# Kernel tuning notes

Measured on AMD Instinct MI355X. Metric: run time of the kernel, lower is better.

## Reference

```python
import jax, jax.numpy as jnp
import numpy as np

WS = 49        # window size
NH = 8         # num heads


def setup_inputs() -> dict:
    key = jax.random.key(0)
    k1, k2, k3 = jax.random.split(key, 3)
    B, N, C = 4, 50176, 512
    x = jax.random.normal(k1, (B, N, C), dtype=jnp.float32)
    w_qkv = jax.random.normal(k2, (3 * C, C), dtype=jnp.float32) * (C ** -0.5)
    b_qkv = jnp.zeros((3 * C,), dtype=jnp.float32)
    w_proj = jax.random.normal(k3, (C, C), dtype=jnp.float32) * (C ** -0.5)
    b_proj = jnp.zeros((C,), dtype=jnp.float32)
    return {"x": x, "w_qkv": w_qkv, "b_qkv": b_qkv, "w_proj": w_proj, "b_proj": b_proj}


def reference(x, w_qkv, b_qkv, w_proj, b_proj):
    B, N, C = x.shape
    w = N // WS
    hd = C // NH
    scale = hd ** -0.5
    # shuffle: 'b (ws w) c -> (b w) ws c'  (outer factor is ws -> strided windows)
    xw = x.reshape(B, WS, w, C).transpose(0, 2, 1, 3).reshape(B * w, WS, C)
    qkv = xw @ w_qkv.T + b_qkv                       # [(B w), WS, 3C]
    qkv = qkv.reshape(B * w, WS, 3, NH, hd)
    q = qkv[:, :, 0].transpose(0, 2, 1, 3) * scale   # [(B w), NH, WS, hd]
    k = qkv[:, :, 1].transpose(0, 2, 1, 3)
    v = qkv[:, :, 2].transpose(0, 2, 1, 3)
    attn = jax.nn.softmax(jnp.einsum('bhqd,bhkd->bhqk', q, k), axis=-1)
    out = jnp.einsum('bhqk,bhkd->bhqd', attn, v)     # [(B w), NH, WS, hd]
    out = out.transpose(0, 2, 1, 3).reshape(B * w, WS, C)
    out = out @ w_proj.T + b_proj
    # unshuffle: '(b w) ws c -> b (ws w) c'
    out = out.reshape(B, w, WS, C).transpose(0, 2, 1, 3).reshape(B, N, C)
    return out
```

## Files before the change

kernel.cpp:

```cpp
#include <hip/hip_runtime.h>
#include <cstdint>
#include <cstddef>


typedef __bf16 bf16x8 __attribute__((ext_vector_type(8)));
typedef __bf16 bf16x4 __attribute__((ext_vector_type(4)));
typedef float  f32x4  __attribute__((ext_vector_type(4)));

#define MFMA_BF16(a, b, c) __builtin_amdgcn_mfma_f32_16x16x32_bf16((a), (b), (c), 0, 0, 0)

static __device__ __forceinline__ int swzi(int row, int col) {
  return col ^ ((row & 7) << 3);
}

typedef __attribute__((address_space(1))) const void gconst_t;
typedef __attribute__((address_space(3))) void lds_t;
static __device__ __forceinline__ void gload16(const void* g, void* l) {
  __builtin_amdgcn_global_load_lds((gconst_t*)g, (lds_t*)l, 16, 0, 0);
}

#define RAW_BAR()  asm volatile("s_barrier" ::: "memory")
#define WAITV(N)   asm volatile("s_waitcnt vmcnt(" #N ")" ::: "memory")

__global__ void prep_weights(const float* __restrict__ wqkv,
                             const float* __restrict__ bqkv,
                             const float* __restrict__ wproj,
                             __bf16* __restrict__ wqkv_bf,
                             __bf16* __restrict__ wproj_bf,
                             float* __restrict__ bq_s) {
  const int stride = gridDim.x * blockDim.x;
  const int t0 = blockIdx.x * blockDim.x + threadIdx.x;
  for (int i = t0; i < 1536 * 512; i += stride) {
    float v = wqkv[i];
    if (i < 512 * 512) v *= 0.125f;
    wqkv_bf[i] = (__bf16)v;
  }
  for (int i = t0; i < 512 * 512; i += stride) wproj_bf[i] = (__bf16)wproj[i];
  for (int i = t0; i < 1536; i += stride)      bq_s[i] = (i < 512 ? 0.125f : 1.0f) * bqkv[i];
}

__global__ void prep_x(const float* __restrict__ x, __bf16* __restrict__ xb) {
  const size_t total  = (size_t)200704 * 512 / 8;
  const size_t stride = (size_t)gridDim.x * blockDim.x;
  for (size_t i = (size_t)blockIdx.x * blockDim.x + threadIdx.x; i < total; i += stride) {
    const float4 a = *(const float4*)(x + i * 8);
    const float4 b = *(const float4*)(x + i * 8 + 4);
    bf16x8 t;
    t[0] = (__bf16)a.x; t[1] = (__bf16)a.y; t[2] = (__bf16)a.z; t[3] = (__bf16)a.w;
    t[4] = (__bf16)b.x; t[5] = (__bf16)b.y; t[6] = (__bf16)b.z; t[7] = (__bf16)b.w;
    *(bf16x8*)(xb + i * 8) = t;
  }
}

template<bool OUT_F32>
__launch_bounds__(512, 1)
__global__ void gemm256(const __bf16* __restrict__ Ab,
                        const __bf16* __restrict__ Bw,
                        const float* __restrict__ bias,
                        void* __restrict__ Cv,
                        int Mtiles, int Ntiles) {
  __shared__ __align__(16) __bf16 sA[2][256 * 64];
  __shared__ __align__(16) __bf16 sB[2][256 * 64];

  const int tid  = threadIdx.x;
  const int lane = tid & 63;
  const int l15  = lane & 15;
  const int kgc  = (lane >> 4) & 3;
  const int r4   = kgc * 4;
  const int wv   = tid >> 6;
  const int wm   = wv >> 2, wn = wv & 3;

  const int nwg = Mtiles * Ntiles;
  const int cpx = nwg >> 3;
  const int wg  = (blockIdx.x & 7) * cpx + (blockIdx.x >> 3);
  const int mt  = wg / Ntiles;
  const int nt  = wg % Ntiles;
  const size_t m0 = (size_t)mt * 256;
  const int    n0 = nt * 256;

  const int srow   = tid >> 3;
  const int schunk = (tid & 7) ^ (srow & 7);

  f32x4 acc[8][4];
  const f32x4 zf = {0.f, 0.f, 0.f, 0.f};
#pragma unroll
  for (int i = 0; i < 8; ++i)
#pragma unroll
    for (int j = 0; j < 4; ++j) acc[i][j] = zf;

  auto STAGE = [&](int bufi, int kt) {
    const size_t kof = (size_t)kt * 64 + schunk * 8;
#pragma unroll
    for (int j = 0; j < 4; ++j) {
      gload16(Ab + (m0 + (size_t)(j * 64 + srow)) * 512 + kof,
              &sA[bufi][0] + j * 4096 + tid * 8);
      gload16(Bw + ((size_t)(n0 + j * 64 + srow)) * 512 + kof,
              &sB[bufi][0] + j * 4096 + tid * 8);
    }
  };

  auto COMPUTE = [&](int bufi) {
#pragma unroll
    for (int ks = 0; ks < 2; ++ks) {
      bf16x8 bfrag[4];
#pragma unroll
      for (int n = 0; n < 4; ++n) {
        const int r = wn * 64 + n * 16 + l15;
        bfrag[n] = *(const bf16x8*)&sB[bufi][r * 64 + (((ks * 4 + kgc) ^ (r & 7)) * 8)];
      }
#pragma unroll
      for (int mh = 0; mh < 2; ++mh) {
        bf16x8 afrag[4];
#pragma unroll
        for (int m2 = 0; m2 < 4; ++m2) {
          const int r = wm * 128 + mh * 64 + m2 * 16 + l15;
          afrag[m2] = *(const bf16x8*)&sA[bufi][r * 64 + (((ks * 4 + kgc) ^ (r & 7)) * 8)];
        }
        __builtin_amdgcn_s_setprio(1);
#pragma unroll
        for (int m2 = 0; m2 < 4; ++m2)
#pragma unroll
          for (int n = 0; n < 4; ++n)
            acc[mh * 4 + m2][n] = MFMA_BF16(afrag[m2], bfrag[n], acc[mh * 4 + m2][n]);
        __builtin_amdgcn_s_setprio(0);
      }
    }
  };

  STAGE(0, 0);

  for (int tt = 0; tt < 8; tt += 2) {
    RAW_BAR();
    STAGE(1, tt + 1);
    WAITV(8);
    RAW_BAR();
    COMPUTE(0);

    RAW_BAR();
    if (tt < 6) {
      STAGE(0, tt + 2);
      WAITV(8);
    } else {
      WAITV(0);
    }
    RAW_BAR();
    COMPUTE(1);
  }

  const int Nld = Ntiles * 256;
#pragma unroll
  for (int n = 0; n < 4; ++n) {
    const int col = n0 + wn * 64 + n * 16 + l15;
    const float bb = bias[col];
#pragma unroll
    for (int m = 0; m < 8; ++m) {
#pragma unroll
      for (int r = 0; r < 4; ++r) {
        const size_t row = m0 + wm * 128 + m * 16 + r4 + r;
        const float v = acc[m][n][r] + bb;
        if (OUT_F32) ((float*)Cv)[row * (size_t)Nld + col] = v;
        else         ((__bf16*)Cv)[row * (size_t)Nld + col] = (__bf16)v;
      }
    }
  }
}

__launch_bounds__(512)
__global__ void attn_win(const __bf16* __restrict__ qkv, __bf16* __restrict__ O) {
  __shared__ __align__(16) __bf16 vT[8 * 64 * 64];
  __shared__ __align__(16) __bf16 sP[8][16 * 64];

  const int tid  = threadIdx.x;
  const int lane = tid & 63;
  const int h    = tid >> 6;
  const int l15  = lane & 15;
  const int kg   = ((lane >> 4) & 3) * 8;
  const int r4   = ((lane >> 4) & 3) * 4;

  const int blk = blockIdx.x;
  const int b   = blk >> 10;
  const int wi  = blk & 1023;
  const size_t tokbase = (size_t)b * 50176 + wi;

  const int MOFF[4] = {0, 16, 32, 33};
  const float NEG_INF = -__builtin_inff();

  bf16x8 aq[4][2], bk[4][2];
#pragma unroll
  for (int mt = 0; mt < 4; ++mt) {
    const size_t tok = tokbase + (size_t)(MOFF[mt] + l15) * 1024;
#pragma unroll
    for (int ks = 0; ks < 2; ++ks) {
      aq[mt][ks] = *(const bf16x8*)(qkv + tok * 1536 +       h * 64 + ks * 32 + kg);
      bk[mt][ks] = *(const bf16x8*)(qkv + tok * 1536 + 512 + h * 64 + ks * 32 + kg);
    }
  }

  for (int i = tid; i < 8 * 64 * 16; i += 512) {
    const int k = 48 + (i & 15);
    if (k != 48) {
      const int n  = (i >> 4) & 63;
      const int hh = i >> 10;
      vT[hh * 4096 + n * 64 + (k ^ ((n & 7) << 3))] = (__bf16)0.0f;
    }
  }
  for (int i = tid; i < 49 * 64; i += 512) {
    const int s  = i >> 6;
    const int c8 = (i & 63) * 8;
    bf16x8 v8 = *(const bf16x8*)(qkv + (tokbase + (size_t)s * 1024) * 1536 + 1024 + c8);
    const int hh = c8 >> 6;
#pragma unroll
    for (int j = 0; j < 8; ++j) {
      const int n = (c8 & 63) + j;
      vT[hh * 4096 + n * 64 + (s ^ ((n & 7) << 3))] = v8[j];
    }
  }
  __syncthreads();

  bf16x8 bv[4][2];
#pragma unroll
  for (int ntv = 0; ntv < 4; ++ntv) {
    const int n = ntv * 16 + l15;
#pragma unroll
    for (int ks = 0; ks < 2; ++ks)
      bv[ntv][ks] = *(const bf16x8*)&vT[h * 4096 + n * 64 + ((ks * 32 + kg) ^ ((n & 7) << 3))];
  }

  f32x4 accS[4][4];
  const f32x4 zf = {0.f, 0.f, 0.f, 0.f};
#pragma unroll
  for (int m = 0; m < 4; ++m)
#pragma unroll
    for (int n = 0; n < 4; ++n) accS[m][n] = zf;
#pragma unroll
  for (int ks = 0; ks < 2; ++ks)
#pragma unroll
    for (int m = 0; m < 4; ++m)
#pragma unroll
      for (int n = 0; n < 4; ++n)
        accS[m][n] = MFMA_BF16(aq[m][ks], bk[n][ks], accS[m][n]);

#pragma unroll
  for (int mt = 0; mt < 4; ++mt) {
#pragma unroll
    for (int r = 0; r < 4; ++r) {
      const int prow = r4 + r;
      const float sv0 = accS[mt][0][r];
      const float sv1 = accS[mt][1][r];
      const float sv2 = accS[mt][2][r];
      const float sv3 = (l15 == 15) ? accS[mt][3][r] : NEG_INF;
      float mx = fmaxf(fmaxf(sv0, sv1), fmaxf(sv2, sv3));
      mx = fmaxf(mx, __shfl_xor(mx, 1));
      mx = fmaxf(mx, __shfl_xor(mx, 2));
      mx = fmaxf(mx, __shfl_xor(mx, 4));
      mx = fmaxf(mx, __shfl_xor(mx, 8));
      const float e0 = __expf(sv0 - mx);
      const float e1 = __expf(sv1 - mx);
      const float e2 = __expf(sv2 - mx);
      const float e3 = __expf(sv3 - mx);
      float sum = e0 + e1 + e2 + e3;
      sum += __shfl_xor(sum, 1);
      sum += __shfl_xor(sum, 2);
      sum += __shfl_xor(sum, 4);
      sum += __shfl_xor(sum, 8);
      const float inv = 1.0f / sum;
      sP[h][prow * 64 + swzi(prow, 0  + l15)] = (__bf16)(e0 * inv);
      sP[h][prow * 64 + swzi(prow, 16 + l15)] = (__bf16)(e1 * inv);
      sP[h][prow * 64 + swzi(prow, 32 + l15)] = (__bf16)(e2 * inv);
      if (l15 == 15) sP[h][prow * 64 + swzi(prow, 48)] = (__bf16)(e3 * inv);
      if (l15 < 15)  sP[h][prow * 64 + swzi(prow, 49 + l15)] = (__bf16)0.0f;
    }
    bf16x8 ap[2];
#pragma unroll
    for (int ks = 0; ks < 2; ++ks)
      ap[ks] = *(const bf16x8*)&sP[h][l15 * 64 + swzi(l15, ks * 32 + kg)];
    f32x4 accO[4];
#pragma unroll
    for (int n = 0; n < 4; ++n) accO[n] = zf;
#pragma unroll
    for (int ks = 0; ks < 2; ++ks)
#pragma unroll
      for (int n = 0; n < 4; ++n)
        accO[n] = MFMA_BF16(ap[ks], bv[n][ks], accO[n]);
#pragma unroll
    for (int n = 0; n < 4; ++n) {
#pragma unroll
      for (int r = 0; r < 4; ++r) {
        const int row = MOFF[mt] + r4 + r;
        O[(tokbase + (size_t)row * 1024) * 512 + h * 64 + n * 16 + l15] =
            (__bf16)accO[n][r];
      }
    }
  }
}

__launch_bounds__(256, 2)
__global__ void swin_attn_fused(const float* __restrict__ x,
                                const __bf16* __restrict__ wqkv_bf,
                                const float* __restrict__ bq_s,
                                const __bf16* __restrict__ wproj_bf,
                                const float* __restrict__ bproj,
                                float* __restrict__ out) {
  __shared__ __align__(16) __bf16 s_xw[49 * 512];
  __shared__ __align__(16) __bf16 s_q [49 * 64];
  __shared__ __align__(16) __bf16 s_k [49 * 64];
  __shared__ __align__(16) __bf16 s_vT[64 * 64];
  __shared__ __align__(16) __bf16 s_p [49 * 64];

  const int tid  = threadIdx.x;
  const int lane = tid & 63;
  const int wv   = tid >> 6;
  const int l15  = lane & 15;
  const int kg   = (lane >> 4) * 8;
  const int r4   = (lane >> 4) * 4;
  const int blk = blockIdx.x;
  const int b   = blk >> 10;
  const int wi  = blk & 1023;
  const int MOFF[4] = {0, 16, 32, 33};
  const float NEG_INF = -__builtin_inff();

  for (int i = tid; i < 64 * 64; i += 256) s_vT[i] = (__bf16)0.0f;
  const float* xwin = x + ((size_t)b * 50176 + (size_t)wi) * 512;
  for (int idx = tid; idx < 49 * 128; idx += 256) {
    const int row = idx >> 7;
    const int c4  = (idx & 127) * 4;
    const float4 v = *(const float4*)(xwin + (size_t)row * (1024 * 512) + c4);
    bf16x4 t;
    t.x = (__bf16)v.x; t.y = (__bf16)v.y; t.z = (__bf16)v.z; t.w = (__bf16)v.w;
    *(bf16x4*)&s_xw[row * 512 + swzi(row, c4)] = t;
  }
  f32x4 accF[4][8];
  const f32x4 zf = {0.f, 0.f, 0.f, 0.f};
#pragma unroll
  for (int m = 0; m < 4; ++m)
#pragma unroll
    for (int n = 0; n < 8; ++n) accF[m][n] = zf;
  __syncthreads();

  for (int h = 0; h < 8; ++h) {
    f32x4 accA[4][3];
#pragma unroll
    for (int m = 0; m < 4; ++m)
#pragma unroll
      for (int n = 0; n < 3; ++n) accA[m][n] = zf;
    const __bf16* pB[3];
    float biasv[3];
#pragma unroll
    for (int nt = 0; nt < 3; ++nt) {
      const int c  = wv * 48 + nt * 16 + l15;
      const int wr = (c < 64) ? (h * 64 + c)
                   : (c < 128) ? (512 + h * 64 + (c - 64))
                               : (1024 + h * 64 + (c - 128));
      pB[nt]    = wqkv_bf + (size_t)wr * 512 + kg;
      biasv[nt] = bq_s[wr];
    }
#pragma unroll
    for (int ks = 0; ks < 16; ++ks) {
      bf16x8 a[4], bb[3];
#pragma unroll
      for (int mt = 0; mt < 4; ++mt) {
        const int row = MOFF[mt] + l15;
        a[mt] = *(const bf16x8*)&s_xw[row * 512 + swzi(row, ks * 32 + kg)];
      }
#pragma unroll
      for (int nt = 0; nt < 3; ++nt) bb[nt] = *(const bf16x8*)(pB[nt] + ks * 32);
#pragma unroll
      for (int mt = 0; mt < 4; ++mt)
#pragma unroll
        for (int nt = 0; nt < 3; ++nt)
          accA[mt][nt] = MFMA_BF16(a[mt], bb[nt], accA[mt][nt]);
    }
#pragma unroll
    for (int nt = 0; nt < 3; ++nt) {
      const int c = wv * 48 + nt * 16 + l15;
#pragma unroll
      for (int mt = 0; mt < 4; ++mt) {
#pragma unroll
        for (int r = 0; r < 4; ++r) {
          const int row = MOFF[mt] + r4 + r;
          const __bf16 bvv = (__bf16)(accA[mt][nt][r] + biasv[nt]);
          if (c < 64)       s_q[row * 64 + swzi(row, c)] = bvv;
          else if (c < 128) s_k[row * 64 + swzi(row, c - 64)] = bvv;
          else {
            const int vr = c - 128;
            s_vT[vr * 64 + swzi(vr, row)] = bvv;
          }
        }
      }
    }
    __syncthreads();

    const int R = MOFF[wv];
    bf16x8 aq[2], bkf[4][2];
#pragma unroll
    for (int ks2 = 0; ks2 < 2; ++ks2) {
      const int row = R + l15;
      aq[ks2] = *(const bf16x8*)&s_q[row * 64 + swzi(row, ks2 * 32 + kg)];
    }
#pragma unroll
    for (int nt = 0; nt < 4; ++nt) {
      const int row = MOFF[nt] + l15;
#pragma unroll
      for (int ks2 = 0; ks2 < 2; ++ks2)
        bkf[nt][ks2] = *(const bf16x8*)&s_k[row * 64 + swzi(row, ks2 * 32 + kg)];
    }
    f32x4 accS[4];
#pragma unroll
    for (int n = 0; n < 4; ++n) accS[n] = zf;
#pragma unroll
    for (int ks2 = 0; ks2 < 2; ++ks2)
#pragma unroll
      for (int nt = 0; nt < 4; ++nt)
        accS[nt] = MFMA_BF16(aq[ks2], bkf[nt][ks2], accS[nt]);
#pragma unroll
    for (int r = 0; r < 4; ++r) {
      const int row = R + r4 + r;
      const float sv0 = accS[0][r];
      const float sv1 = accS[1][r];
      const float sv2 = accS[2][r];
      const float sv3 = (l15 == 15) ? accS[3][r] : NEG_INF;
      float m = fmaxf(fmaxf(sv0, sv1), fmaxf(sv2, sv3));
      m = fmaxf(m, __shfl_xor(m, 1));
      m = fmaxf(m, __shfl_xor(m, 2));
      m = fmaxf(m, __shfl_xor(m, 4));
      m = fmaxf(m, __shfl_xor(m, 8));
      const float e0 = __expf(sv0 - m);
      const float e1 = __expf(sv1 - m);
      const float e2 = __expf(sv2 - m);
      const float e3 = __expf(sv3 - m);
      float s = e0 + e1 + e2 + e3;
      s += __shfl_xor(s, 1);
      s += __shfl_xor(s, 2);
      s += __shfl_xor(s, 4);
      s += __shfl_xor(s, 8);
      const float inv = 1.0f / s;
      s_p[row * 64 + swzi(row, 0  + l15)] = (__bf16)(e0 * inv);
      s_p[row * 64 + swzi(row, 16 + l15)] = (__bf16)(e1 * inv);
      s_p[row * 64 + swzi(row, 32 + l15)] = (__bf16)(e2 * inv);
      if (l15 == 15) s_p[row * 64 + swzi(row, 48)] = (__bf16)(e3 * inv);
      if (l15 < 15)  s_p[row * 64 + swzi(row, 49 + l15)] = (__bf16)0.0f;
    }
    bf16x8 ap[2], bv2[4][2];
#pragma unroll
    for (int ks2 = 0; ks2 < 2; ++ks2) {
      const int row = R + l15;
      ap[ks2] = *(const bf16x8*)&s_p[row * 64 + swzi(row, ks2 * 32 + kg)];
    }
#pragma unroll
    for (int nt = 0; nt < 4; ++nt) {
      const int row = nt * 16 + l15;
#pragma unroll
      for (int ks2 = 0; ks2 < 2; ++ks2)
        bv2[nt][ks2] = *(const bf16x8*)&s_vT[row * 64 + swzi(row, ks2 * 32 + kg)];
    }
    __syncthreads();
    f32x4 accO[4];
#pragma unroll
    for (int n = 0; n < 4; ++n) accO[n] = zf;
#pragma unroll
    for (int ks2 = 0; ks2 < 2; ++ks2)
#pragma unroll
      for (int nt = 0; nt < 4; ++nt)
        accO[nt] = MFMA_BF16(ap[ks2], bv2[nt][ks2], accO[nt]);
#pragma unroll
    for (int nt = 0; nt < 4; ++nt) {
#pragma unroll
      for (int r = 0; r < 4; ++r) {
        const int row = R + r4 + r;
        s_p[row * 64 + swzi(row, nt * 16 + l15)] = (__bf16)accO[nt][r];
      }
    }
    __syncthreads();
#pragma unroll
    for (int ks2 = 0; ks2 < 2; ++ks2) {
      bf16x8 ao[4], bw[8];
#pragma unroll
      for (int mt = 0; mt < 4; ++mt) {
        const int row = MOFF[mt] + l15;
        ao[mt] = *(const bf16x8*)&s_p[row * 64 + swzi(row, ks2 * 32 + kg)];
      }
#pragma unroll
      for (int nt = 0; nt < 8; ++nt) {
        const int cc = wv * 128 + nt * 16 + l15;
        bw[nt] = *(const bf16x8*)(wproj_bf + (size_t)cc * 512 + h * 64 + ks2 * 32 + kg);
      }
#pragma unroll
      for (int mt = 0; mt < 4; ++mt)
#pragma unroll
        for (int nt = 0; nt < 8; ++nt)
          accF[mt][nt] = MFMA_BF16(ao[mt], bw[nt], accF[mt][nt]);
    }
  }
#pragma unroll
  for (int nt = 0; nt < 8; ++nt) {
    const int cc = wv * 128 + nt * 16 + l15;
    const float bp = bproj[cc];
#pragma unroll
    for (int mt = 0; mt < 4; ++mt) {
#pragma unroll
      for (int r = 0; r < 4; ++r) {
        const int row = MOFF[mt] + r4 + r;
        if (mt < 3 || (r4 + r) == 15) {
          out[((size_t)b * 50176 + (size_t)row * 1024 + (size_t)wi) * 512 + cc] =
              accF[mt][nt][r] + bp;
        }
      }
    }
  }
}

extern "C" void kernel_launch(void* const* d_in, const int* in_sizes, int n_in,
                              void* d_out, int out_size, void* d_ws, size_t ws_size,
                              hipStream_t stream) {
  const float* x      = (const float*)d_in[0];
  const float* w_qkv  = (const float*)d_in[1];
  const float* b_qkv  = (const float*)d_in[2];
  const float* w_proj = (const float*)d_in[3];
  const float* b_proj = (const float*)d_in[4];
  float* outp = (float*)d_out;

  const size_t QKV_E = (size_t)200704 * 1536;
  const size_t O_E   = (size_t)200704 * 512;
  const size_t NEED  = (QKV_E + O_E + 786432 + 262144) * 2 + 1536 * 4;

  if (ws_size >= NEED) {
    __bf16* qkv      = (__bf16*)d_ws;
    __bf16* Obuf     = qkv + QKV_E;
    __bf16* wqkv_bf  = Obuf + O_E;
    __bf16* wproj_bf = wqkv_bf + 786432;
    float*  bq_s     = (float*)(wproj_bf + 262144);

    prep_weights<<<512, 256, 0, stream>>>(w_qkv, b_qkv, w_proj, wqkv_bf, wproj_bf, bq_s);
    prep_x<<<2048, 256, 0, stream>>>(x, Obuf);
    gemm256<false><<<784 * 6, 512, 0, stream>>>(Obuf, wqkv_bf, bq_s, qkv, 784, 6);
    attn_win<<<4096, 512, 0, stream>>>(qkv, Obuf);
    gemm256<true ><<<784 * 2, 512, 0, stream>>>(Obuf, wproj_bf, b_proj, outp, 784, 2);
  } else {
    __bf16* wqkv_bf  = (__bf16*)d_ws;
    __bf16* wproj_bf = wqkv_bf + 1536 * 512;
    float*  bq_s     = (float*)(wproj_bf + 512 * 512);
    prep_weights<<<1024, 256, 0, stream>>>(w_qkv, b_qkv, w_proj, wqkv_bf, wproj_bf, bq_s);
    swin_attn_fused<<<4096, 256, 0, stream>>>(x, wqkv_bf, bq_s, wproj_bf, b_proj, outp);
  }
}
```

Measured before the change: 1.138 ms.

## Restructure GEMM main loop into barrier-synchronized quarter phases with two blocks per CU

Replaces the two-buffer unrolled K loop with a single loop that splits each K tile into four phases (LDS fragment loads, barrier, MFMA burst, barrier), issuing the next tile's global-to-LDS stage at the start of the first phase. Waits for all outstanding loads at each tile start instead of using partial vmcnt waits. It also raises launch bounds to request two 512-thread blocks per CU so warps from different blocks can overlap. The changes aim to interleave memory and MFMA work across waves more evenly, at the cost of more barriers and register pressure that may not allow two blocks to fit given the 64KB LDS footprint.

```diff
diff --git a/kernel.cpp b/kernel.cpp
--- a/kernel.cpp
+++ b/kernel.cpp
@@ -19,8 +19,7 @@
   __builtin_amdgcn_global_load_lds((gconst_t*)g, (lds_t*)l, 16, 0, 0);
 }
 
-#define RAW_BAR()  asm volatile("s_barrier" ::: "memory")
-#define WAITV(N)   asm volatile("s_waitcnt vmcnt(" #N ")" ::: "memory")
+#define WAITV0()   asm volatile("s_waitcnt vmcnt(0)" ::: "memory")
 
 __global__ void prep_weights(const float* __restrict__ wqkv,
                              const float* __restrict__ bqkv,
@@ -53,7 +52,7 @@
 }
 
 template<bool OUT_F32>
-__launch_bounds__(512, 1)
+__launch_bounds__(512, 2)
 __global__ void gemm256(const __bf16* __restrict__ Ab,
                         const __bf16* __restrict__ Bw,
                         const float* __restrict__ bias,
@@ -99,53 +98,54 @@
     }
   };
 
-  auto COMPUTE = [&](int bufi) {
-#pragma unroll
-    for (int ks = 0; ks < 2; ++ks) {
-      bf16x8 bfrag[4];
-#pragma unroll
-      for (int n = 0; n < 4; ++n) {
-        const int r = wn * 64 + n * 16 + l15;
-        bfrag[n] = *(const bf16x8*)&sB[bufi][r * 64 + (((ks * 4 + kgc) ^ (r & 7)) * 8)];
-      }
-#pragma unroll
-      for (int mh = 0; mh < 2; ++mh) {
-        bf16x8 afrag[4];
-#pragma unroll
-        for (int m2 = 0; m2 < 4; ++m2) {
-          const int r = wm * 128 + mh * 64 + m2 * 16 + l15;
-          afrag[m2] = *(const bf16x8*)&sA[bufi][r * 64 + (((ks * 4 + kgc) ^ (r & 7)) * 8)];
-        }
-        __builtin_amdgcn_s_setprio(1);
-#pragma unroll
-        for (int m2 = 0; m2 < 4; ++m2)
-#pragma unroll
-          for (int n = 0; n < 4; ++n)
-            acc[mh * 4 + m2][n] = MFMA_BF16(afrag[m2], bfrag[n], acc[mh * 4 + m2][n]);
-        __builtin_amdgcn_s_setprio(0);
-      }
-    }
-  };
+#define QPHASE(KS, MH, DO_B, DO_STAGE)                                        \
+  {                                                                           \
+    if ((DO_STAGE) && t < 7) STAGE(nxt, t + 1);                               \
+    if (DO_B) {                                                               \
+      _Pragma("unroll")                                                       \
+      for (int n = 0; n < 4; ++n) {                                           \
+        const int r = wn * 64 + n * 16 + l15;                                 \
+        bfrag[n] = *(const bf16x8*)&sB[buf][r * 64 +                          \
+                     ((((KS) * 4 + kgc) ^ (r & 7)) * 8)];                     \
+      }                                                                       \
+    }                                                                         \
+    bf16x8 afrag[4];                                                          \
+    _Pragma("unroll")                                                         \
+    for (int m2 = 0; m2 < 4; ++m2) {                                          \
+      const int r = wm * 128 + (MH) * 64 + m2 * 16 + l15;                     \
+      afrag[m2] = *(const bf16x8*)&sA[buf][r * 64 +                           \
+                    ((((KS) * 4 + kgc) ^ (r & 7)) * 8)];                      \
+    }                                                                         \
+    __builtin_amdgcn_s_barrier();                                             \
+    __builtin_amdgcn_sched_barrier(0);                                        \
+    __builtin_amdgcn_s_setprio(1);                                            \
+    _Pragma("unroll")                                                         \
+    for (int m2 = 0; m2 < 4; ++m2)                                            \
+      _Pragma("unroll")                                                       \
+      for (int n = 0; n < 4; ++n)                                             \
+        acc[(MH) * 4 + m2][n] =                                               \
+            MFMA_BF16(afrag[m2], bfrag[n], acc[(MH) * 4 + m2][n]);            \
+    __builtin_amdgcn_s_setprio(0);                                            \
+    __builtin_amdgcn_s_barrier();                                             \
+    __builtin_amdgcn_sched_barrier(0);                                        \
+  }
 
   STAGE(0, 0);
 
-  for (int tt = 0; tt < 8; tt += 2) {
-    RAW_BAR();
-    STAGE(1, tt + 1);
-    WAITV(8);
-    RAW_BAR();
-    COMPUTE(0);
-
-    RAW_BAR();
-    if (tt < 6) {
-      STAGE(0, tt + 2);
-      WAITV(8);
-    } else {
-      WAITV(0);
-    }
-    RAW_BAR();
-    COMPUTE(1);
-  }
+  int buf = 0;
+  for (int t = 0; t < 8; ++t) {
+    const int nxt = buf ^ 1;
+    WAITV0();
+    __builtin_amdgcn_s_barrier();
+    __builtin_amdgcn_sched_barrier(0);
+    bf16x8 bfrag[4];
+    QPHASE(0, 0, 1, 1)
+    QPHASE(0, 1, 0, 0)
+    QPHASE(1, 0, 1, 0)
+    QPHASE(1, 1, 0, 0)
+    buf = nxt;
+  }
+#undef QPHASE
 
   const int Nld = Ntiles * 256;
 #pragma unroll
```

After: 1.240 ms. 9.0% more time.
